# Kernel tuning notes

Hardware: AMD Instinct MI355X
Metric: run time of the kernel (lower is better)

The kernel has to match this reference:

```python
import jax, jax.numpy as jnp
import numpy as np

P, Q = 3, 0
DIM = 1 << (P + Q)  # 8 blades, bitmask-indexed: 1,e1,e2,e3,e12,e13,e23,e123
EPS = 1e-6


def _cayley(p, q):
    """Cayley tensor C[i,j,k]: e_i * e_j = sum_k C[i,j,k] e_k for Cl(p,q)."""
    n = p + q
    dim = 1 << n
    C = np.zeros((dim, dim, dim), dtype=np.float32)
    for a in range(dim):
        for b in range(dim):
            # sign from reordering basis vectors into canonical order
            s = 1
            aa = a >> 1
            while aa:
                if bin(aa & b).count('1') & 1:
                    s = -s
                aa >>= 1
            # metric signs from squared shared basis vectors (negative for q part)
            shared = a & b
            for i in range(n):
                if (shared >> i) & 1 and i >= p:
                    s = -s
            C[a, b, a ^ b] = s
    return jnp.asarray(C)

CAYLEY = _cayley(P, Q)
# reversion sign per blade: (-1)^{g(g-1)/2}, g = grade = popcount(bitmask)
REV = jnp.asarray([(-1.0) ** ((bin(k).count('1') * (bin(k).count('1') - 1)) // 2)
                   for k in range(DIM)], dtype=jnp.float32)

B, CH = 131072, 16


def setup_inputs() -> dict:
    key = jax.random.key(0)
    k1, k2, k3 = jax.random.split(key, 3)
    x = jax.random.normal(k1, (B, CH, DIM), dtype=jnp.float32)
    ln_scale = jnp.ones((CH,), dtype=jnp.float32)
    rotor = jax.random.normal(k2, (CH, DIM), dtype=jnp.float32)
    w = jax.random.normal(k3, (CH, CH, DIM), dtype=jnp.float32) / np.sqrt(CH * DIM)
    bias = jnp.zeros((CH, DIM), dtype=jnp.float32)
    return {"x": x, "ln_scale": ln_scale, "rotor": rotor, "w": w, "bias": bias}


def reference(x, ln_scale, rotor, w, bias):
    # CliffordLayerNorm: normalize each channel's multivector by its blade norm
    n = jnp.sqrt(jnp.sum(x * x, axis=-1, keepdims=True) + EPS)  # [B,C,1]
    x = x / n * ln_scale[None, :, None]
    # RotorLayer: unit rotor per channel, sandwich product R x ~R via Cayley
    r = rotor / jnp.sqrt(jnp.sum(rotor * rotor, axis=-1, keepdims=True) + EPS)  # [C,8]
    r_rev = r * REV[None, :]
    t = jnp.einsum('ci,bcj,ijk->bck', r, x, CAYLEY)      # R * x
    x = jnp.einsum('bci,cj,ijk->bck', t, r_rev, CAYLEY)  # (R*x) * ~R
    # GeometricGELU: per-blade exact GELU
    x = jax.nn.gelu(x, approximate=False)
    # CliffordLinear: multivector-valued weights, geometric-product contraction
    out = jnp.einsum('oci,bcj,ijk->bok', w, x, CAYLEY) + bias[None]
    return out
```

## Files before the change

kernel.cpp:

```cpp
#include <hip/hip_runtime.h>
#include <math.h>
#include <stdint.h>

#define CH 16
#define DIM 8
#define ROW 128
#define TILE_ROWS 64
#define TPB 2
#define BLK 256

typedef __attribute__((ext_vector_type(8))) short bf16x8;
typedef __attribute__((ext_vector_type(4))) float f32x4;
typedef __attribute__((ext_vector_type(4))) unsigned int u32x4;

__device__ __forceinline__ float csign(int a, int b) {
    int s = 0;
    int aa = a >> 1;
    while (aa) { s ^= (__popc(aa & b) & 1); aa >>= 1; }
    return s ? -1.0f : 1.0f;
}

__device__ __forceinline__ unsigned short f2bf(float f) {
    union { float f; unsigned u; } x; x.f = f;
    unsigned r = x.u + 0x7FFF + ((x.u >> 16) & 1);
    return (unsigned short)(r >> 16);
}

__device__ __forceinline__ float gelu_poly(float s) {
    const float z = s * 0.70710678f;
    const float u = z * z;
    float p = -8.5483270e-04f;
    p = fmaf(p, u,  5.2239776e-03f);
    p = fmaf(p, u, -2.6866138e-02f);
    p = fmaf(p, u,  1.1283792e-01f);
    p = fmaf(p, u, -3.7612639e-01f);
    p = fmaf(p, u,  1.1283792e+00f);
    return 0.5f * s * fmaf(z, p, 1.0f);
}

__device__ __forceinline__ void gload_lds16(const float* g, const float* l) {
    __builtin_amdgcn_global_load_lds(
        (const __attribute__((address_space(1))) void*)(uintptr_t)g,
        (__attribute__((address_space(3))) void*)(uint32_t)(uintptr_t)l,
        16, 0, 0);
}

__device__ __forceinline__ void barrier_lgkm() {
    asm volatile("s_waitcnt lgkmcnt(0)" ::: "memory");
    __builtin_amdgcn_s_barrier();
    __builtin_amdgcn_sched_barrier(0);
}
__device__ __forceinline__ void barrier_vm0() {
    asm volatile("s_waitcnt vmcnt(0) lgkmcnt(0)" ::: "memory");
    __builtin_amdgcn_s_barrier();
    __builtin_amdgcn_sched_barrier(0);
}

__global__ void precompute_kernel(const float* __restrict__ rotor,
                                  const float* __restrict__ w,
                                  const float* __restrict__ ln_scale,
                                  float* __restrict__ ws)
{
    const int t = threadIdx.x;
    unsigned short* D   = (unsigned short*)ws;
    unsigned short* w2r = D + 16384;

    ((u32x4*)D)[t]        = (u32x4){0u, 0u, 0u, 0u};
    ((u32x4*)D)[t + 1024] = (u32x4){0u, 0u, 0u, 0u};
    __syncthreads();

    if (t < CH) {
        const int c = t;
        float r[8];
        float nn = 0.f;
        #pragma unroll
        for (int i = 0; i < 8; ++i) { r[i] = rotor[c * 8 + i]; nn += r[i] * r[i]; }
        const float inv = rsqrtf(nn + 1e-6f);
        #pragma unroll
        for (int i = 0; i < 8; ++i) r[i] *= inv;

        const float REVv[8] = {1.f, 1.f, 1.f, -1.f, 1.f, -1.f, -1.f, -1.f};
        float rr[8];
        #pragma unroll
        for (int j = 0; j < 8; ++j) rr[j] = r[j] * REVv[j];

        float L[8][8], R[8][8];
        #pragma unroll
        for (int a = 0; a < 8; ++a)
            #pragma unroll
            for (int b = 0; b < 8; ++b) { L[a][b] = 0.f; R[a][b] = 0.f; }

        #pragma unroll
        for (int i = 0; i < 8; ++i)
            #pragma unroll
            for (int j = 0; j < 8; ++j) {
                const float s = csign(i, j);
                L[i ^ j][j] += r[i] * s;
                R[i ^ j][i] += rr[j] * s;
            }

        const float sc = ln_scale[c];
        #pragma unroll
        for (int k = 0; k < 8; ++k)
            #pragma unroll
            for (int m = 0; m < 8; ++m) {
                float acc = 0.f;
                #pragma unroll
                for (int i = 0; i < 8; ++i) acc += R[k][i] * L[i][m];
                D[(c * 8 + k) * ROW + (c * 8 + m)] = f2bf(acc * sc);
            }
    }

    #pragma unroll
    for (int task = t; task < ROW * CH; task += 1024) {
        const int outf = task >> 4;
        const int ci   = task & 15;
        const int kb = outf & 7, o = outf >> 3;
        const float4 w0 = *(const float4*)(w + (o * CH + ci) * 8);
        const float4 w1 = *(const float4*)(w + (o * CH + ci) * 8 + 4);
        const float wv[8] = {w0.x, w0.y, w0.z, w0.w, w1.x, w1.y, w1.z, w1.w};
        bf16x8 pk;
        #pragma unroll
        for (int j = 0; j < 8; ++j) {
            const int i = kb ^ j;
            pk[j] = (short)f2bf(wv[i] * csign(i, j));
        }
        *(bf16x8*)(w2r + outf * ROW + ci * 8) = pk;
    }
}


__device__ __forceinline__ void prefetch_tile(const float* xt, float* sX,
                                              int wave, int lane) {
    const int dbase = wave * 512 + lane;
    #pragma unroll
    for (int i = 0; i < 8; ++i) {
        const int d  = dbase + i * 64;
        const int r  = d >> 5;
        const int gc = (d & 31) ^ (r & 7);
        gload_lds16(xt + r * ROW + gc * 4, sX + (wave * 512 + i * 64) * 4);
    }
}

__device__ __forceinline__ void phase1_mv(const float4 a, const float4 b,
                                          const bf16x8* Df, unsigned short* sG,
                                          int wave, int lcol, int lkg, int rt) {
    const float nn = a.x*a.x + a.y*a.y + a.z*a.z + a.w*a.w
                   + b.x*b.x + b.y*b.y + b.z*b.z + b.w*b.w;
    const float inv = rsqrtf(nn + 1e-6f);
    bf16x8 af;
    af[0] = (short)f2bf(a.x * inv); af[1] = (short)f2bf(a.y * inv);
    af[2] = (short)f2bf(a.z * inv); af[3] = (short)f2bf(a.w * inv);
    af[4] = (short)f2bf(b.x * inv); af[5] = (short)f2bf(b.y * inv);
    af[6] = (short)f2bf(b.z * inv); af[7] = (short)f2bf(b.w * inv);

    f32x4 p0 = (f32x4){0.f, 0.f, 0.f, 0.f};
    f32x4 p1 = (f32x4){0.f, 0.f, 0.f, 0.f};
    p0 = __builtin_amdgcn_mfma_f32_16x16x32_bf16(af, Df[0], p0, 0, 0, 0);
    p1 = __builtin_amdgcn_mfma_f32_16x16x32_bf16(af, Df[1], p1, 0, 0, 0);

    #pragma unroll
    for (int ctl = 0; ctl < 2; ++ctl) {
        const f32x4 p = ctl ? p1 : p0;
        const int colg = (2 * wave + ctl) * 16 + lcol;
        #pragma unroll
        for (int j = 0; j < 4; ++j) {
            const float y = gelu_poly(p[j]);
            const int row   = rt * 16 + lkg * 4 + j;
            const int chunk = (colg >> 3) ^ (row & 15);
            sG[row * ROW + chunk * 8 + (colg & 7)] = f2bf(y);
        }
    }
}

__device__ __forceinline__ void gemm_tile(const unsigned short* sG,
                                          const bf16x8 Bf[2][4],
                                          f32x4 (&acc)[4][2], int lcol, int lkg) {
    #pragma unroll
    for (int rt = 0; rt < 4; ++rt)
        #pragma unroll
        for (int ct = 0; ct < 2; ++ct)
            acc[rt][ct] = (f32x4){0.f, 0.f, 0.f, 0.f};

    #pragma unroll
    for (int rt = 0; rt < 4; ++rt) {
        const int row = rt * 16 + lcol;
        #pragma unroll
        for (int ks = 0; ks < 4; ++ks) {
            const int chunk = (ks * 4 + lkg) ^ (row & 15);
            const bf16x8 afr = *(const bf16x8*)(sG + row * ROW + chunk * 8);
            acc[rt][0] = __builtin_amdgcn_mfma_f32_16x16x32_bf16(
                             afr, Bf[0][ks], acc[rt][0], 0, 0, 0);
            acc[rt][1] = __builtin_amdgcn_mfma_f32_16x16x32_bf16(
                             afr, Bf[1][ks], acc[rt][1], 0, 0, 0);
        }
    }
}

__device__ __forceinline__ void store_tile(float* out, size_t trow0,
                                           const f32x4 (&acc)[4][2],
                                           int colb, int lcol, int lkg,
                                           const float bv[2]) {
    #pragma unroll
    for (int rt = 0; rt < 4; ++rt) {
        const size_t rbase = trow0 + rt * 16 + lkg * 4;
        #pragma unroll
        for (int ct = 0; ct < 2; ++ct) {
            const int col = colb + ct * 16 + lcol;
            #pragma unroll
            for (int j = 0; j < 4; ++j)
                out[(rbase + j) * ROW + col] = acc[rt][ct][j] + bv[ct];
        }
    }
}

__global__ __launch_bounds__(BLK, 4) void fused_kernel(
        const float* __restrict__ x,
        const float* __restrict__ bias,
        const float* __restrict__ ws,
        float* __restrict__ out)
{
    __shared__ unsigned short sG[TILE_ROWS * ROW];
    __shared__ float sX[TILE_ROWS * ROW];

    const int t    = threadIdx.x;
    const int lane = t & 63;
    const int wave = t >> 6;
    const int lcol = lane & 15;
    const int lkg  = lane >> 4;
    const int c    = 4 * wave + lkg;

    const unsigned short* D   = (const unsigned short*)ws;
    const unsigned short* w2r = D + 16384;

    const size_t row0 = (size_t)blockIdx.x * (TPB * TILE_ROWS);

    float4 xa[4], xb[4];
    #pragma unroll
    for (int rt = 0; rt < 4; ++rt) {
        const float4* xp = (const float4*)(x + ((row0 + rt * 16 + lcol) * CH + c) * DIM);
        xa[rt] = xp[0];
        xb[rt] = xp[1];
    }

    bf16x8 Df[2];
    #pragma unroll
    for (int ctl = 0; ctl < 2; ++ctl) {
        const int col = (2 * wave + ctl) * 16 + lcol;
        Df[ctl] = *(const bf16x8*)(D + col * ROW + 32 * wave + lkg * 8);
    }

    prefetch_tile(x + (row0 + TILE_ROWS) * ROW, sX, wave, lane);

    const int colb = wave * 32;
    bf16x8 Bf[2][4];
    #pragma unroll
    for (int ct = 0; ct < 2; ++ct)
        #pragma unroll
        for (int ks = 0; ks < 4; ++ks) {
            const int col = colb + ct * 16 + lcol;
            Bf[ct][ks] = *(const bf16x8*)(w2r + col * ROW + ks * 32 + lkg * 8);
        }
    float bv[2];
    bv[0] = bias[colb + lcol];
    bv[1] = bias[colb + 16 + lcol];

    #pragma unroll
    for (int rt = 0; rt < 4; ++rt)
        phase1_mv(xa[rt], xb[rt], Df, sG, wave, lcol, lkg, rt);

    barrier_lgkm();

    f32x4 acc[4][2];
    gemm_tile(sG, Bf, acc, lcol, lkg);

    barrier_vm0();

    store_tile(out, row0, acc, colb, lcol, lkg, bv);

    #pragma unroll
    for (int rt = 0; rt < 4; ++rt) {
        const int row = rt * 16 + lcol;
        const int sw  = row & 7;
        const float4 a = *(const float4*)(sX + row * ROW + (((2 * c)     ^ sw) << 2));
        const float4 b = *(const float4*)(sX + row * ROW + (((2 * c + 1) ^ sw) << 2));
        phase1_mv(a, b, Df, sG, wave, lcol, lkg, rt);
    }

    barrier_lgkm();

    gemm_tile(sG, Bf, acc, lcol, lkg);

    store_tile(out, row0 + TILE_ROWS, acc, colb, lcol, lkg, bv);
}

extern "C" void kernel_launch(void* const* d_in, const int* in_sizes, int n_in,
                              void* d_out, int out_size, void* d_ws, size_t ws_size,
                              hipStream_t stream)
{
    const float* x        = (const float*)d_in[0];
    const float* ln_scale = (const float*)d_in[1];
    const float* rotor    = (const float*)d_in[2];
    const float* w        = (const float*)d_in[3];
    const float* bias     = (const float*)d_in[4];
    float* out = (float*)d_out;
    float* ws  = (float*)d_ws;

    precompute_kernel<<<dim3(1), dim3(1024), 0, stream>>>(rotor, w, ln_scale, ws);

    const int nrows   = in_sizes[0] / (CH * DIM);
    const int nblocks = nrows / (TPB * TILE_ROWS);

    fused_kernel<<<dim3(nblocks), dim3(BLK), 0, stream>>>(x, bias, ws, out);
}
```

Measured before the change: 37.51 us.

## Replace LDS async prefetch with register prefetch and double-buffered sG

The second tile's x data is now loaded straight into registers at kernel start instead of through global_load_lds into a float LDS buffer. The sG staging buffer is double-buffered, which removes the vm wait barrier between the first GEMM and the second phase. The precompute kernel is split across two blocks (rotor matrices and weight repack), and store loops are reordered. This cuts LDS use and one barrier, at the cost of more registers for the prefetched x values and possible occupancy pressure.

```diff
diff --git a/kernel.cpp b/kernel.cpp
--- a/kernel.cpp
+++ b/kernel.cpp
@@ -38,20 +38,8 @@
     return 0.5f * s * fmaf(z, p, 1.0f);
 }
 
-__device__ __forceinline__ void gload_lds16(const float* g, const float* l) {
-    __builtin_amdgcn_global_load_lds(
-        (const __attribute__((address_space(1))) void*)(uintptr_t)g,
-        (__attribute__((address_space(3))) void*)(uint32_t)(uintptr_t)l,
-        16, 0, 0);
-}
-
 __device__ __forceinline__ void barrier_lgkm() {
     asm volatile("s_waitcnt lgkmcnt(0)" ::: "memory");
-    __builtin_amdgcn_s_barrier();
-    __builtin_amdgcn_sched_barrier(0);
-}
-__device__ __forceinline__ void barrier_vm0() {
-    asm volatile("s_waitcnt vmcnt(0) lgkmcnt(0)" ::: "memory");
     __builtin_amdgcn_s_barrier();
     __builtin_amdgcn_sched_barrier(0);
 }
@@ -65,82 +53,72 @@
     unsigned short* D   = (unsigned short*)ws;
     unsigned short* w2r = D + 16384;
 
-    ((u32x4*)D)[t]        = (u32x4){0u, 0u, 0u, 0u};
-    ((u32x4*)D)[t + 1024] = (u32x4){0u, 0u, 0u, 0u};
-    __syncthreads();
-
-    if (t < CH) {
-        const int c = t;
-        float r[8];
-        float nn = 0.f;
-        #pragma unroll
-        for (int i = 0; i < 8; ++i) { r[i] = rotor[c * 8 + i]; nn += r[i] * r[i]; }
-        const float inv = rsqrtf(nn + 1e-6f);
-        #pragma unroll
-        for (int i = 0; i < 8; ++i) r[i] *= inv;
-
-        const float REVv[8] = {1.f, 1.f, 1.f, -1.f, 1.f, -1.f, -1.f, -1.f};
-        float rr[8];
-        #pragma unroll
-        for (int j = 0; j < 8; ++j) rr[j] = r[j] * REVv[j];
-
-        float L[8][8], R[8][8];
-        #pragma unroll
-        for (int a = 0; a < 8; ++a)
-            #pragma unroll
-            for (int b = 0; b < 8; ++b) { L[a][b] = 0.f; R[a][b] = 0.f; }
-
-        #pragma unroll
-        for (int i = 0; i < 8; ++i)
+    if (blockIdx.x == 0) {
+        ((u32x4*)D)[t]        = (u32x4){0u, 0u, 0u, 0u};
+        ((u32x4*)D)[t + 1024] = (u32x4){0u, 0u, 0u, 0u};
+        __syncthreads();
+
+        if (t < CH) {
+            const int c = t;
+            float r[8];
+            float nn = 0.f;
+            #pragma unroll
+            for (int i = 0; i < 8; ++i) { r[i] = rotor[c * 8 + i]; nn += r[i] * r[i]; }
+            const float inv = rsqrtf(nn + 1e-6f);
+            #pragma unroll
+            for (int i = 0; i < 8; ++i) r[i] *= inv;
+
+            const float REVv[8] = {1.f, 1.f, 1.f, -1.f, 1.f, -1.f, -1.f, -1.f};
+            float rr[8];
+            #pragma unroll
+            for (int j = 0; j < 8; ++j) rr[j] = r[j] * REVv[j];
+
+            float L[8][8], R[8][8];
+            #pragma unroll
+            for (int a = 0; a < 8; ++a)
+                #pragma unroll
+                for (int b = 0; b < 8; ++b) { L[a][b] = 0.f; R[a][b] = 0.f; }
+
+            #pragma unroll
+            for (int i = 0; i < 8; ++i)
+                #pragma unroll
+                for (int j = 0; j < 8; ++j) {
+                    const float s = csign(i, j);
+                    L[i ^ j][j] += r[i] * s;
+                    R[i ^ j][i] += rr[j] * s;
+                }
+
+            const float sc = ln_scale[c];
+            #pragma unroll
+            for (int k = 0; k < 8; ++k)
+                #pragma unroll
+                for (int m = 0; m < 8; ++m) {
+                    float acc = 0.f;
+                    #pragma unroll
+                    for (int i = 0; i < 8; ++i) acc += R[k][i] * L[i][m];
+                    D[(c * 8 + k) * ROW + (c * 8 + m)] = f2bf(acc * sc);
+                }
+        }
+    } else {
+        #pragma unroll
+        for (int task = t; task < ROW * CH; task += 1024) {
+            const int outf = task >> 4;
+            const int ci   = task & 15;
+            const int kb = outf & 7, o = outf >> 3;
+            const float4 w0 = *(const float4*)(w + (o * CH + ci) * 8);
+            const float4 w1 = *(const float4*)(w + (o * CH + ci) * 8 + 4);
+            const float wv[8] = {w0.x, w0.y, w0.z, w0.w, w1.x, w1.y, w1.z, w1.w};
+            bf16x8 pk;
             #pragma unroll
             for (int j = 0; j < 8; ++j) {
-                const float s = csign(i, j);
-                L[i ^ j][j] += r[i] * s;
-                R[i ^ j][i] += rr[j] * s;
+                const int i = kb ^ j;
+                pk[j] = (short)f2bf(wv[i] * csign(i, j));
             }
-
-        const float sc = ln_scale[c];
-        #pragma unroll
-        for (int k = 0; k < 8; ++k)
-            #pragma unroll
-            for (int m = 0; m < 8; ++m) {
-                float acc = 0.f;
-                #pragma unroll
-                for (int i = 0; i < 8; ++i) acc += R[k][i] * L[i][m];
-                D[(c * 8 + k) * ROW + (c * 8 + m)] = f2bf(acc * sc);
-            }
-    }
-
-    #pragma unroll
-    for (int task = t; task < ROW * CH; task += 1024) {
-        const int outf = task >> 4;
-        const int ci   = task & 15;
-        const int kb = outf & 7, o = outf >> 3;
-        const float4 w0 = *(const float4*)(w + (o * CH + ci) * 8);
-        const float4 w1 = *(const float4*)(w + (o * CH + ci) * 8 + 4);
-        const float wv[8] = {w0.x, w0.y, w0.z, w0.w, w1.x, w1.y, w1.z, w1.w};
-        bf16x8 pk;
-        #pragma unroll
-        for (int j = 0; j < 8; ++j) {
-            const int i = kb ^ j;
-            pk[j] = (short)f2bf(wv[i] * csign(i, j));
-        }
-        *(bf16x8*)(w2r + outf * ROW + ci * 8) = pk;
-    }
-}
-
-
-__device__ __forceinline__ void prefetch_tile(const float* xt, float* sX,
-                                              int wave, int lane) {
-    const int dbase = wave * 512 + lane;
-    #pragma unroll
-    for (int i = 0; i < 8; ++i) {
-        const int d  = dbase + i * 64;
-        const int r  = d >> 5;
-        const int gc = (d & 31) ^ (r & 7);
-        gload_lds16(xt + r * ROW + gc * 4, sX + (wave * 512 + i * 64) * 4);
-    }
-}
+            *(bf16x8*)(w2r + outf * ROW + ci * 8) = pk;
+        }
+    }
+}
+
 
 __device__ __forceinline__ void phase1_mv(const float4 a, const float4 b,
                                           const bf16x8* Df, unsigned short* sG,
@@ -205,11 +183,12 @@
     for (int rt = 0; rt < 4; ++rt) {
         const size_t rbase = trow0 + rt * 16 + lkg * 4;
         #pragma unroll
-        for (int ct = 0; ct < 2; ++ct) {
-            const int col = colb + ct * 16 + lcol;
-            #pragma unroll
-            for (int j = 0; j < 4; ++j)
+        for (int j = 0; j < 4; ++j) {
+            #pragma unroll
+            for (int ct = 0; ct < 2; ++ct) {
+                const int col = colb + ct * 16 + lcol;
                 out[(rbase + j) * ROW + col] = acc[rt][ct][j] + bv[ct];
+            }
         }
     }
 }
@@ -220,8 +199,7 @@
         const float* __restrict__ ws,
         float* __restrict__ out)
 {
-    __shared__ unsigned short sG[TILE_ROWS * ROW];
-    __shared__ float sX[TILE_ROWS * ROW];
+    __shared__ unsigned short sG[2][TILE_ROWS * ROW];
 
     const int t    = threadIdx.x;
     const int lane = t & 63;
@@ -235,12 +213,12 @@
 
     const size_t row0 = (size_t)blockIdx.x * (TPB * TILE_ROWS);
 
-    float4 xa[4], xb[4];
+    float4 xa0[4], xb0[4];
     #pragma unroll
     for (int rt = 0; rt < 4; ++rt) {
         const float4* xp = (const float4*)(x + ((row0 + rt * 16 + lcol) * CH + c) * DIM);
-        xa[rt] = xp[0];
-        xb[rt] = xp[1];
+        xa0[rt] = xp[0];
+        xb0[rt] = xp[1];
     }
 
     bf16x8 Df[2];
@@ -249,9 +227,6 @@
         const int col = (2 * wave + ctl) * 16 + lcol;
         Df[ctl] = *(const bf16x8*)(D + col * ROW + 32 * wave + lkg * 8);
     }
-
-    prefetch_tile(x + (row0 + TILE_ROWS) * ROW, sX, wave, lane);
-
     const int colb = wave * 32;
     bf16x8 Bf[2][4];
     #pragma unroll
@@ -265,32 +240,31 @@
     bv[0] = bias[colb + lcol];
     bv[1] = bias[colb + 16 + lcol];
 
+    float4 xa1[4], xb1[4];
+    #pragma unroll
+    for (int rt = 0; rt < 4; ++rt) {
+        const float4* xp = (const float4*)(x + ((row0 + TILE_ROWS + rt * 16 + lcol) * CH + c) * DIM);
+        xa1[rt] = xp[0];
+        xb1[rt] = xp[1];
+    }
+
     #pragma unroll
     for (int rt = 0; rt < 4; ++rt)
-        phase1_mv(xa[rt], xb[rt], Df, sG, wave, lcol, lkg, rt);
+        phase1_mv(xa0[rt], xb0[rt], Df, sG[0], wave, lcol, lkg, rt);
 
     barrier_lgkm();
 
     f32x4 acc[4][2];
-    gemm_tile(sG, Bf, acc, lcol, lkg);
-
-    barrier_vm0();
-
+    gemm_tile(sG[0], Bf, acc, lcol, lkg);
     store_tile(out, row0, acc, colb, lcol, lkg, bv);
 
     #pragma unroll
-    for (int rt = 0; rt < 4; ++rt) {
-        const int row = rt * 16 + lcol;
-        const int sw  = row & 7;
-        const float4 a = *(const float4*)(sX + row * ROW + (((2 * c)     ^ sw) << 2));
-        const float4 b = *(const float4*)(sX + row * ROW + (((2 * c + 1) ^ sw) << 2));
-        phase1_mv(a, b, Df, sG, wave, lcol, lkg, rt);
-    }
+    for (int rt = 0; rt < 4; ++rt)
+        phase1_mv(xa1[rt], xb1[rt], Df, sG[1], wave, lcol, lkg, rt);
 
     barrier_lgkm();
 
-    gemm_tile(sG, Bf, acc, lcol, lkg);
-
+    gemm_tile(sG[1], Bf, acc, lcol, lkg);
     store_tile(out, row0 + TILE_ROWS, acc, colb, lcol, lkg, bv);
 }
 
@@ -306,7 +280,7 @@
     float* out = (float*)d_out;
     float* ws  = (float*)d_ws;
 
-    precompute_kernel<<<dim3(1), dim3(1024), 0, stream>>>(rotor, w, ln_scale, ws);
+    precompute_kernel<<<dim3(2), dim3(1024), 0, stream>>>(rotor, w, ln_scale, ws);
 
     const int nrows   = in_sizes[0] / (CH * DIM);
     const int nblocks = nrows / (TPB * TILE_ROWS);
```

After: 34.79 us. 1.08x faster.
